# Kernel optimization log

Hardware: AMD Instinct MI355X
Metric: run time of the kernel (lower is better)

## Reference

```python
import jax, jax.numpy as jnp
import numpy as np

B, G, N1, S1 = 2, 16, 4096, 1024
D1, D2 = 128, 256
IN_CH = D1 + D2
MLP = [256, 256]
EPS_DIST = 1e-8
EPS_BN = 1e-5


def setup_inputs() -> dict:
    key = jax.random.key(0)
    ks = jax.random.split(key, 6)
    return {
        "xyz1": jax.random.normal(ks[0], (B, 3, G * N1), jnp.float32),
        "points1": jax.random.normal(ks[1], (B, D1, G * N1), jnp.float32),
        "point_split1": jnp.arange(G + 1, dtype=jnp.int32) * N1,
        "xyz2": jax.random.normal(ks[2], (B, 3, G * S1), jnp.float32),
        "points2": jax.random.normal(ks[3], (B, D2, G * S1), jnp.float32),
        "point_split2": jnp.arange(G + 1, dtype=jnp.int32) * S1,
        "W1": jax.random.normal(ks[4], (MLP[0], IN_CH), jnp.float32) / np.sqrt(IN_CH).astype(np.float32),
        "b1": jnp.zeros((MLP[0],), jnp.float32),
        "gamma1": jnp.ones((MLP[0],), jnp.float32),
        "beta1": jnp.zeros((MLP[0],), jnp.float32),
        "W2": jax.random.normal(ks[5], (MLP[1], MLP[0]), jnp.float32) / np.sqrt(MLP[0]).astype(np.float32),
        "b2": jnp.zeros((MLP[1],), jnp.float32),
        "gamma2": jnp.ones((MLP[1],), jnp.float32),
        "beta2": jnp.zeros((MLP[1],), jnp.float32),
    }


def _bn_relu(x, gamma, beta):
    # training-mode BatchNorm1d over (batch, points) per channel; x: [B, C, N]
    mu = x.mean(axis=(0, 2), keepdims=True)
    var = x.var(axis=(0, 2), keepdims=True)  # biased var, as torch training BN
    xn = (x - mu) * jax.lax.rsqrt(var + EPS_BN)
    return jax.nn.relu(xn * gamma[None, :, None] + beta[None, :, None])


def _fp_segment(x1, x2, p1, p2, W1, b1, g1, be1, W2, b2, g2, be2):
    # x1 [B,3,n], x2 [B,3,s], p1 [B,D1,n], p2 [B,D2,s]
    d = jnp.sum((x1[:, :, :, None] - x2[:, :, None, :]) ** 2, axis=1)  # [B,n,s]
    negd, idx = jax.lax.top_k(-d, 3)  # 3 nearest neighbors
    w = 1.0 / (-negd + EPS_DIST)
    w = w / jnp.sum(w, axis=-1, keepdims=True)  # [B,n,3]

    def gather(p2b, ixb, wb):  # [D2,s], [n,3], [n,3] -> [D2,n]
        return jnp.einsum('dnk,nk->dn', p2b[:, ixb], wb)

    interp = jax.vmap(gather)(p2, idx, w)  # [B,D2,n]
    h = jnp.concatenate([p1, interp], axis=1)  # [B,IN_CH,n]
    h = _bn_relu(jnp.einsum('oc,bcn->bon', W1, h) + b1[None, :, None], g1, be1)
    h = _bn_relu(jnp.einsum('oc,bcn->bon', W2, h) + b2[None, :, None], g2, be2)
    return h  # [B, MLP[-1], n]


def _forward(xyz1, points1, xyz2, points2, W1, b1, gamma1, beta1, W2, b2, gamma2, beta2, g):
    n1 = xyz1.shape[-1] // g
    s1 = xyz2.shape[-1] // g
    seg = lambda t, L: jnp.moveaxis(t.reshape(t.shape[0], t.shape[1], g, L), 2, 0)  # -> [G,B,C,L]
    out = jax.vmap(_fp_segment, in_axes=(0, 0, 0, 0) + (None,) * 8)(
        seg(xyz1, n1), seg(xyz2, s1), seg(points1, n1), seg(points2, s1),
        W1, b1, gamma1, beta1, W2, b2, gamma2, beta2)  # [G,B,C,n1]
    return jnp.moveaxis(out, 0, 2).reshape(out.shape[1], out.shape[2], g * n1)  # [B,C,N]


def reference(xyz1, points1, point_split1, xyz2, points2, point_split2,
              W1, b1, gamma1, beta1, W2, b2, gamma2, beta2):
    g = point_split1.shape[0] - 1  # number of ragged segments (uniform here)
    return _forward(xyz1, points1, xyz2, points2, W1, b1, gamma1, beta1,
                    W2, b2, gamma2, beta2, g)
```

## Files before the change

### kernel.cpp

```cpp
#include <hip/hip_runtime.h>
#include <hip/hip_bf16.h>
#include <hip/hip_fp16.h>

#define B_    2
#define G_    16
#define N_    4096
#define S_    1024
#define D1_   128
#define D2_   256
#define CIN_  384
#define BG_   32
#define GN_   65536
#define GS_   16384

typedef unsigned int u32;
typedef unsigned short u16;
typedef _Float16 f16x8 __attribute__((ext_vector_type(8)));
typedef float f32x4 __attribute__((ext_vector_type(4)));

__device__ __forceinline__ u32 h2bits(__half2 h) { union { __half2 h; u32 u; } c; c.h = h; return c.u; }
__device__ __forceinline__ __half2 bits2h(u32 u) { union { __half2 h; u32 u; } c; c.u = u; return c.h; }
__device__ __forceinline__ u32 pkmax0(u32 v) {
  u32 r; asm("v_pk_max_f16 %0, %1, %2" : "=v"(r) : "v"(v), "v"(0)); return r;
}

#define OFF_W1PK   0u
#define OFF_W2PK   196608u
#define OFF_XYZ2P  327680u
#define OFF_SUM1   851968u
#define OFF_SQ1    868352u
#define OFF_SUM2   884736u
#define OFF_SQ2    901120u
#define OFF_SCPK1  917504u
#define OFF_SHPK1  925696u
#define OFF_SS2    950272u
#define OFF_KNNP   983040u
#define OFF_P2T    5177344u
#define OFF_Y2     21954560u
#define OFF_Y1     122617856u

__launch_bounds__(256)
__global__ void prep_kernel(const float* __restrict__ W1, const float* __restrict__ W2,
                            const float* __restrict__ xyz2,
                            u16* __restrict__ W1pk, u16* __restrict__ W2pk,
                            float4* __restrict__ xyz2p, float* __restrict__ zeros)
{
  int idx = blockIdx.x * 256 + threadIdx.x;
  if (idx < 12288) {
    int lane = idx & 63, ks = (idx >> 6) % 12, mr = idx / (64 * 12);
    int m = mr * 16 + (lane & 15), k = ks * 32 + (lane >> 4) * 8;
    const float* src = W1 + (size_t)m * 384 + k;
    u16* dst = W1pk + (size_t)idx * 8;
    #pragma unroll
    for (int e = 0; e < 8; e++) dst[e] = __half_as_ushort(__float2half_rn(src[e]));
    return;
  }
  idx -= 12288;
  if (idx < 8192) {
    int lane = idx & 63, ks = (idx >> 6) % 8, mr = idx / (64 * 8);
    int m = mr * 16 + (lane & 15), k = ks * 32 + (lane >> 4) * 8;
    const float* src = W2 + (size_t)m * 256 + k;
    u16* dst = W2pk + (size_t)idx * 8;
    #pragma unroll
    for (int e = 0; e < 8; e++) dst[e] = __half_as_ushort(__float2half_rn(src[e]));
    return;
  }
  idx -= 8192;
  if (idx < 16384) { zeros[idx] = 0.f; return; }
  idx -= 16384;
  int bg = idx >> 8, q = idx & 255;
  int b = bg >> 4, g = bg & 15;
  const float* base = xyz2 + (size_t)b * 3 * GS_ + (size_t)g * S_ + q * 4;
  float4 X = *(const float4*)(base);
  float4 Y = *(const float4*)(base + GS_);
  float4 Z = *(const float4*)(base + 2 * GS_);
  float4 M;
  M.x = X.x*X.x + Y.x*Y.x + Z.x*Z.x;
  M.y = X.y*X.y + Y.y*Y.y + Z.y*Z.y;
  M.z = X.z*X.z + Y.z*Y.z + Z.z*Z.z;
  M.w = X.w*X.w + Y.w*Y.w + Z.w*Z.w;
  float4* dst = xyz2p + (size_t)idx * 4;
  dst[0] = X; dst[1] = Y; dst[2] = Z; dst[3] = M;
}

__launch_bounds__(256)
__global__ void t2_kernel(const float* __restrict__ p2, u16* __restrict__ p2T)
{
  __shared__ float tl[64][65];
  int bx = blockIdx.x;
  int bg = bx >> 6, r = bx & 63;
  int ct = r >> 4, st = r & 15;
  int c0 = ct * 64, s0 = st * 64;
  int b = bg >> 4, g = bg & 15;
  int t = threadIdx.x, lane = t & 63, w = t >> 6;
  const float* src = p2 + (size_t)b * D2_ * GS_ + (size_t)g * S_ + s0 + lane;
  #pragma unroll
  for (int i = 0; i < 16; i++) {
    int row = w * 16 + i;
    tl[row][lane] = src[(size_t)(c0 + row) * GS_];
  }
  __syncthreads();
  int cp = t & 31, sr = t >> 5;
  #pragma unroll
  for (int i = 0; i < 8; i++) {
    int sl = sr * 8 + i;
    u32 v = h2bits(__floats2half2_rn(tl[2 * cp][sl], tl[2 * cp + 1][sl]));
    *(u32*)(p2T + (((size_t)bg * 1024 + s0 + sl) * 256 + c0 + 2 * cp)) = v;
  }
}

__launch_bounds__(256)
__global__ void knn_kernel(const float* __restrict__ xyz1, const float4* __restrict__ xyz2p,
                           uint4* __restrict__ knnp)
{
  __shared__ float sd[3][256];
  __shared__ int si[3][256];
  int bx = blockIdx.x;
  int bg = bx >> 6, blk = bx & 63;
  int b = bg >> 4, g = bg & 15;
  int t = threadIdx.x;
  int lane = t & 63, w = t >> 6;
  int n = blk * 64 + lane;
  const float* x1b = xyz1 + (size_t)b * 3 * GN_ + (size_t)g * N_ + n;
  float x = x1b[0], y = x1b[GN_], z = x1b[2 * GN_];
  const float4* xp = xyz2p + (size_t)bg * 1024;

  float d0 = 3.4e38f, d1 = 3.4e38f, d2 = 3.4e38f;
  int i0 = 0, i1 = 0, i2 = 0;
  for (int qq = 0; qq < 64; qq++) {
    int q = w * 64 + qq;
    float4 X = xp[q * 4 + 0], Y = xp[q * 4 + 1], Z = xp[q * 4 + 2], M = xp[q * 4 + 3];
    const float* Xa = (const float*)&X;
    const float* Ya = (const float*)&Y;
    const float* Za = (const float*)&Z;
    const float* Ma = (const float*)&M;
    #pragma unroll
    for (int u = 0; u < 4; u++) {
      float cr = x * Xa[u];
      cr = fmaf(y, Ya[u], cr);
      cr = fmaf(z, Za[u], cr);
      float d = fmaf(-2.f, cr, Ma[u]);
      int s = q * 4 + u;
      bool c2 = d < d2, c1 = d < d1, c0 = d < d0;
      d2 = c1 ? d1 : (c2 ? d : d2);  i2 = c1 ? i1 : (c2 ? s : i2);
      d1 = c0 ? d0 : (c1 ? d : d1);  i1 = c0 ? i0 : (c1 ? s : i1);
      d0 = c0 ? d : d0;              i0 = c0 ? s : i0;
    }
  }

  sd[0][t] = d0; sd[1][t] = d1; sd[2][t] = d2;
  si[0][t] = i0; si[1][t] = i1; si[2][t] = i2;
  __syncthreads();

  if (t < 64) {
    float D0 = d0, D1 = d1, D2 = d2;
    int I0 = i0, I1 = i1, I2 = i2;
    #pragma unroll
    for (int qtr = 1; qtr < 4; qtr++) {
      int idx = qtr * 64 + t;
      #pragma unroll
      for (int c = 0; c < 3; c++) {
        float d = sd[c][idx];
        int s = si[c][idx];
        bool c0 = d < D0, c1 = d < D1, c2 = d < D2;
        I2 = c1 ? I1 : (c2 ? s : I2);  D2 = c1 ? D1 : (c2 ? d : D2);
        I1 = c0 ? I0 : (c1 ? s : I1);  D1 = c0 ? D0 : (c1 ? d : D1);
        I0 = c0 ? s : I0;              D0 = c0 ? d : D0;
      }
    }
    float m1 = x * x + y * y + z * z;
    float t0 = fmaxf(D0 + m1, 0.f), t1 = fmaxf(D1 + m1, 0.f), t2v = fmaxf(D2 + m1, 0.f);
    float w0 = 1.f / (t0 + 1e-8f);
    float w1 = 1.f / (t1 + 1e-8f);
    float w2 = 1.f / (t2v + 1e-8f);
    float inv = 1.f / (w0 + w1 + w2);
    uint4 rec;
    rec.x = h2bits(__floats2half2_rn(w0 * inv, w1 * inv));
    rec.y = (u32)__half_as_ushort(__float2half_rn(w2 * inv));
    rec.z = (u32)I0 | ((u32)I1 << 16);
    rec.w = (u32)I2;
    knnp[(size_t)bg * 4096 + n] = rec;
  }
}

__launch_bounds__(512, 6)
__global__ void gemm1_kernel(const u16* __restrict__ W1pk, const float* __restrict__ points1,
                             const u16* __restrict__ p2T, const uint4* __restrict__ knnp,
                             const float* __restrict__ bias,
                             float* __restrict__ sumw, float* __restrict__ sqw,
                             u16* __restrict__ Y1)
{
  __shared__ __align__(16) char smem[49152];
  int bx = blockIdx.x;
  int bg = bx >> 6, nt = bx & 63;
  int b = bg >> 4, g = bg & 15;
  int n0 = nt * 64;
  int t = threadIdx.x, wid = t >> 6, l = t & 63;
  int llo = l & 15, lhi = l >> 4;

  {
    int r = t >> 3, c4 = t & 7;
    size_t kb = (size_t)bg * 4096 + n0;
    const u16* p2b = p2T + (size_t)bg * 1024 * 256;
    uint4 kp = knnp[kb + r];
    __half2 w0 = __half2half2(__low2half(bits2h(kp.x)));
    __half2 w1 = __half2half2(__high2half(bits2h(kp.x)));
    __half2 w2 = __half2half2(__low2half(bits2h(kp.y)));
    int i0 = kp.z & 0xffff, i1 = kp.z >> 16, i2 = kp.w & 0xffff;
    const u16* r0 = p2b + (size_t)i0 * 256;
    const u16* r1 = p2b + (size_t)i1 * 256;
    const u16* r2 = p2b + (size_t)i2 * 256;
    #pragma unroll
    for (int u = 0; u < 4; u++) {
      int ch = c4 + 8 * u;
      uint4 q0 = *(const uint4*)(r0 + ch * 8);
      uint4 q1 = *(const uint4*)(r1 + ch * 8);
      uint4 q2 = *(const uint4*)(r2 + ch * 8);
      const u32* a0 = (const u32*)&q0;
      const u32* a1 = (const u32*)&q1;
      const u32* a2 = (const u32*)&q2;
      uint4 o;
      u32* ow = (u32*)&o;
      #pragma unroll
      for (int w = 0; w < 4; w++) {
        __half2 v = __hmul2(w2, bits2h(a2[w]));
        v = __hfma2(w1, bits2h(a1[w]), v);
        v = __hfma2(w0, bits2h(a0[w]), v);
        ow[w] = h2bits(v);
      }
      *(uint4*)(smem + r * 768 + ((256 + ch * 16) ^ ((r & 15) << 4))) = o;
    }
    int row = t & 63, chgrp = t >> 6;
    const float* p1c = points1 + ((size_t)b * 128 + chgrp * 16) * (size_t)GN_
                     + (size_t)g * N_ + n0 + row;
    #pragma unroll
    for (int cp = 0; cp < 8; cp++) {
      int c = chgrp * 16 + cp * 2;
      u32 pk = h2bits(__floats2half2_rn(p1c[(size_t)(cp * 2) * GN_],
                                        p1c[(size_t)(cp * 2 + 1) * GN_]));
      *(u32*)(smem + row * 768 + ((c * 2) ^ ((row & 15) << 4))) = pk;
    }
  }
  __syncthreads();

  f32x4 acc[2][4];
  #pragma unroll
  for (int i = 0; i < 2; i++)
    #pragma unroll
    for (int j = 0; j < 4; j++) acc[i][j] = (f32x4)0.f;

  for (int ks = 0; ks < 12; ks++) {
    f16x8 bfr[4], afr[2];
    #pragma unroll
    for (int i = 0; i < 2; i++)
      afr[i] = *(const f16x8*)(W1pk + (size_t)(((wid * 2 + i) * 12 + ks) * 64 + l) * 8);
    #pragma unroll
    for (int j = 0; j < 4; j++) {
      int rb = j * 16 + llo;
      bfr[j] = *(const f16x8*)(smem + rb * 768 + ((ks * 64 + lhi * 16) ^ ((rb & 15) << 4)));
    }
    #pragma unroll
    for (int i = 0; i < 2; i++)
      #pragma unroll
      for (int j = 0; j < 4; j++)
        acc[i][j] = __builtin_amdgcn_mfma_f32_16x16x32_f16(afr[i], bfr[j], acc[i][j], 0, 0, 0);
  }
  __syncthreads();

  #pragma unroll
  for (int i = 0; i < 2; i++) {
    int mloc = wid * 32 + i * 16 + lhi * 4;
    float b0 = bias[mloc], b1 = bias[mloc + 1], b2 = bias[mloc + 2], b3 = bias[mloc + 3];
    float s0 = 0, s1 = 0, s2 = 0, s3 = 0, q0 = 0, q1 = 0, q2 = 0, q3 = 0;
    int slotb = (mloc * 2) & ~15, off8 = (mloc * 2) & 15;
    #pragma unroll
    for (int j = 0; j < 4; j++) {
      int n = j * 16 + llo;
      float v0 = acc[i][j][0] + b0;
      float v1 = acc[i][j][1] + b1;
      float v2 = acc[i][j][2] + b2;
      float v3 = acc[i][j][3] + b3;
      s0 += v0; q0 += v0 * v0;
      s1 += v1; q1 += v1 * v1;
      s2 += v2; q2 += v2 * v2;
      s3 += v3; q3 += v3 * v3;
      int base = n * 512 + (slotb ^ ((n & 7) << 4)) + off8;
      *(u32*)(smem + base) = h2bits(__floats2half2_rn(v0, v1));
      *(u32*)(smem + base + 4) = h2bits(__floats2half2_rn(v2, v3));
    }
    #pragma unroll
    for (int off = 1; off < 16; off <<= 1) {
      s0 += __shfl_xor(s0, off, 64); q0 += __shfl_xor(q0, off, 64);
      s1 += __shfl_xor(s1, off, 64); q1 += __shfl_xor(q1, off, 64);
      s2 += __shfl_xor(s2, off, 64); q2 += __shfl_xor(q2, off, 64);
      s3 += __shfl_xor(s3, off, 64); q3 += __shfl_xor(q3, off, 64);
    }
    if (llo == 0) {
      atomicAdd(&sumw[g * 256 + mloc], s0);     atomicAdd(&sqw[g * 256 + mloc], q0);
      atomicAdd(&sumw[g * 256 + mloc + 1], s1); atomicAdd(&sqw[g * 256 + mloc + 1], q1);
      atomicAdd(&sumw[g * 256 + mloc + 2], s2); atomicAdd(&sqw[g * 256 + mloc + 2], q2);
      atomicAdd(&sumw[g * 256 + mloc + 3], s3); atomicAdd(&sqw[g * 256 + mloc + 3], q3);
    }
  }
  __syncthreads();
  {
    int rn = t >> 3, cq = t & 7;
    u16* yrow = Y1 + ((size_t)bg * 4096 + n0 + rn) * 256;
    #pragma unroll
    for (int u = 0; u < 4; u++) {
      int s = u * 8 + cq;
      uint4 v = *(const uint4*)(smem + rn * 512 + ((s * 16) ^ ((rn & 7) << 4)));
      *(uint4*)(yrow + s * 8) = v;
    }
  }
}

__global__ void bnfin_kernel(const float* __restrict__ sum, const float* __restrict__ sq,
                             const float* __restrict__ gamma, const float* __restrict__ beta,
                             float2* __restrict__ ss, u32* __restrict__ scpk, u32* __restrict__ shpk)
{
  __shared__ float scl[256], shl[256];
  int g = blockIdx.x, m = threadIdx.x;
  int i = g * 256 + m;
  float mean = sum[i] * (1.f / 8192.f);
  float var = sq[i] * (1.f / 8192.f) - mean * mean;
  var = fmaxf(var, 0.f);
  float rstd = rsqrtf(var + 1e-5f);
  float sc = gamma[m] * rstd;
  float sh = beta[m] - mean * sc;
  if (ss) ss[i] = make_float2(sc, sh);
  if (scpk) {
    scl[m] = sc; shl[m] = sh;
    __syncthreads();
    if (m < 128) {
      scpk[g * 128 + m] = h2bits(__floats2half2_rn(scl[2 * m], scl[2 * m + 1]));
      shpk[g * 128 + m] = h2bits(__floats2half2_rn(shl[2 * m], shl[2 * m + 1]));
    }
  }
}

__launch_bounds__(512, 6)
__global__ void gemm2_kernel(const u16* __restrict__ W2pk, const u16* __restrict__ Y1,
                             const u32* __restrict__ scpk, const u32* __restrict__ shpk,
                             const float* __restrict__ bias,
                             float* __restrict__ sumw, float* __restrict__ sqw,
                             u16* __restrict__ Y2)
{
  __shared__ __align__(16) char smem[33792];
  int bx = blockIdx.x;
  int bg = bx >> 6, nt = bx & 63;
  int b = bg >> 4, g = bg & 15;
  int n0 = nt * 64;
  int t = threadIdx.x, wid = t >> 6, l = t & 63;
  int llo = l & 15, lhi = l >> 4;

  if (t < 128) {
    *(u32*)(smem + 32768 + t * 4) = scpk[g * 128 + t];
    *(u32*)(smem + 33280 + t * 4) = shpk[g * 128 + t];
  }

  {
    int rn = t >> 3, qq = t & 7;
    const u16* yrow = Y1 + ((size_t)bg * 4096 + n0 + rn) * 256;
    uint4 sreg[4];
    #pragma unroll
    for (int u = 0; u < 4; u++) sreg[u] = *(const uint4*)(yrow + (qq * 4 + u) * 8);
    __syncthreads();
    const u32* scp = (const u32*)(smem + 32768);
    const u32* shp = (const u32*)(smem + 33280);
    #pragma unroll
    for (int u = 0; u < 4; u++) {
      int s = qq * 4 + u;
      const u32* yw = (const u32*)&sreg[u];
      uint4 o;
      u32* ow = (u32*)&o;
      #pragma unroll
      for (int w = 0; w < 4; w++) {
        int pairi = s * 4 + w;
        __half2 v = __hfma2(bits2h(yw[w]), bits2h(scp[pairi]), bits2h(shp[pairi]));
        ow[w] = pkmax0(h2bits(v));
      }
      *(uint4*)(smem + rn * 512 + ((s * 16) ^ ((rn & 15) << 4))) = o;
    }
  }
  __syncthreads();

  f32x4 acc[2][4];
  #pragma unroll
  for (int i = 0; i < 2; i++)
    #pragma unroll
    for (int j = 0; j < 4; j++) acc[i][j] = (f32x4)0.f;

  for (int ks = 0; ks < 8; ks++) {
    f16x8 bfr[4], afr[2];
    #pragma unroll
    for (int i = 0; i < 2; i++)
      afr[i] = *(const f16x8*)(W2pk + (size_t)(((wid * 2 + i) * 8 + ks) * 64 + l) * 8);
    #pragma unroll
    for (int j = 0; j < 4; j++) {
      int rb = j * 16 + llo;
      bfr[j] = *(const f16x8*)(smem + rb * 512 + ((ks * 64 + lhi * 16) ^ ((rb & 15) << 4)));
    }
    #pragma unroll
    for (int i = 0; i < 2; i++)
      #pragma unroll
      for (int j = 0; j < 4; j++)
        acc[i][j] = __builtin_amdgcn_mfma_f32_16x16x32_f16(afr[i], bfr[j], acc[i][j], 0, 0, 0);
  }
  __syncthreads();

  #pragma unroll
  for (int i = 0; i < 2; i++) {
    int mloc = wid * 32 + i * 16 + lhi * 4;
    float b0 = bias[mloc], b1 = bias[mloc + 1], b2 = bias[mloc + 2], b3 = bias[mloc + 3];
    float s0 = 0, s1 = 0, s2 = 0, s3 = 0, q0 = 0, q1 = 0, q2 = 0, q3 = 0;
    #pragma unroll
    for (int j = 0; j < 4; j++) {
      int n = j * 16 + llo;
      int slotn = (n >> 3) * 16, offn = (n * 2) & 15;
      float v0 = acc[i][j][0] + b0;
      float v1 = acc[i][j][1] + b1;
      float v2 = acc[i][j][2] + b2;
      float v3 = acc[i][j][3] + b3;
      s0 += v0; q0 += v0 * v0;
      s1 += v1; q1 += v1 * v1;
      s2 += v2; q2 += v2 * v2;
      s3 += v3; q3 += v3 * v3;
      *(u16*)(smem + (mloc + 0) * 128 + (slotn ^ (((mloc + 0) & 7) << 4)) + offn) =
          __half_as_ushort(__float2half_rn(v0));
      *(u16*)(smem + (mloc + 1) * 128 + (slotn ^ (((mloc + 1) & 7) << 4)) + offn) =
          __half_as_ushort(__float2half_rn(v1));
      *(u16*)(smem + (mloc + 2) * 128 + (slotn ^ (((mloc + 2) & 7) << 4)) + offn) =
          __half_as_ushort(__float2half_rn(v2));
      *(u16*)(smem + (mloc + 3) * 128 + (slotn ^ (((mloc + 3) & 7) << 4)) + offn) =
          __half_as_ushort(__float2half_rn(v3));
    }
    #pragma unroll
    for (int off = 1; off < 16; off <<= 1) {
      s0 += __shfl_xor(s0, off, 64); q0 += __shfl_xor(q0, off, 64);
      s1 += __shfl_xor(s1, off, 64); q1 += __shfl_xor(q1, off, 64);
      s2 += __shfl_xor(s2, off, 64); q2 += __shfl_xor(q2, off, 64);
      s3 += __shfl_xor(s3, off, 64); q3 += __shfl_xor(q3, off, 64);
    }
    if (llo == 0) {
      atomicAdd(&sumw[g * 256 + mloc], s0);     atomicAdd(&sqw[g * 256 + mloc], q0);
      atomicAdd(&sumw[g * 256 + mloc + 1], s1); atomicAdd(&sqw[g * 256 + mloc + 1], q1);
      atomicAdd(&sumw[g * 256 + mloc + 2], s2); atomicAdd(&sqw[g * 256 + mloc + 2], q2);
      atomicAdd(&sumw[g * 256 + mloc + 3], s3); atomicAdd(&sqw[g * 256 + mloc + 3], q3);
    }
  }
  __syncthreads();
  {
    int mr = t >> 1, hh = t & 1;
    u16* yrow = Y2 + ((size_t)b * 256 + mr) * (size_t)GN_ + (size_t)g * N_ + n0;
    #pragma unroll
    for (int u = 0; u < 4; u++) {
      int s = hh * 4 + u;
      uint4 v = *(const uint4*)(smem + mr * 128 + ((s * 16) ^ ((mr & 7) << 4)));
      *(uint4*)(yrow + s * 8) = v;
    }
  }
}

__launch_bounds__(256)
__global__ void bnapply2_kernel(const u16* __restrict__ Y2, const float2* __restrict__ ss,
                                float* __restrict__ Out)
{
  int f8 = blockIdx.x * 256 + threadIdx.x;
  size_t base = (size_t)f8 * 8;
  int m = (int)((base >> 16) & 255);
  int g = (int)((base >> 12) & 15);
  float2 sc = ss[g * 256 + m];
  uint4 yv = *(const uint4*)(Y2 + base);
  const u32* yw = (const u32*)&yv;
  float4 a, b4;
  float* av = (float*)&a;
  float* bvv = (float*)&b4;
  #pragma unroll
  for (int i = 0; i < 2; i++) {
    float2 f = __half22float2(bits2h(yw[i]));
    av[2 * i]     = fmaxf(fmaf(f.x, sc.x, sc.y), 0.f);
    av[2 * i + 1] = fmaxf(fmaf(f.y, sc.x, sc.y), 0.f);
  }
  #pragma unroll
  for (int i = 0; i < 2; i++) {
    float2 f = __half22float2(bits2h(yw[2 + i]));
    bvv[2 * i]     = fmaxf(fmaf(f.x, sc.x, sc.y), 0.f);
    bvv[2 * i + 1] = fmaxf(fmaf(f.y, sc.x, sc.y), 0.f);
  }
  *(float4*)(Out + base) = a;
  *(float4*)(Out + base + 4) = b4;
}

extern "C" void kernel_launch(void* const* d_in, const int* in_sizes, int n_in,
                              void* d_out, int out_size, void* d_ws, size_t ws_size,
                              hipStream_t stream)
{
  (void)in_sizes; (void)n_in; (void)out_size; (void)ws_size;
  const float* xyz1    = (const float*)d_in[0];
  const float* points1 = (const float*)d_in[1];
  const float* xyz2    = (const float*)d_in[3];
  const float* points2 = (const float*)d_in[4];
  const float* W1      = (const float*)d_in[6];
  const float* b1      = (const float*)d_in[7];
  const float* gamma1  = (const float*)d_in[8];
  const float* beta1   = (const float*)d_in[9];
  const float* W2      = (const float*)d_in[10];
  const float* b2      = (const float*)d_in[11];
  const float* gamma2  = (const float*)d_in[12];
  const float* beta2   = (const float*)d_in[13];
  float* out = (float*)d_out;
  char* ws = (char*)d_ws;

  u16*    W1pk  = (u16*)(ws + OFF_W1PK);
  u16*    W2pk  = (u16*)(ws + OFF_W2PK);
  float4* xyz2p = (float4*)(ws + OFF_XYZ2P);
  float*  sum1  = (float*)(ws + OFF_SUM1);
  float*  sq1   = (float*)(ws + OFF_SQ1);
  float*  sum2  = (float*)(ws + OFF_SUM2);
  float*  sq2   = (float*)(ws + OFF_SQ2);
  u32*    scpk1 = (u32*)(ws + OFF_SCPK1);
  u32*    shpk1 = (u32*)(ws + OFF_SHPK1);
  float2* ss2   = (float2*)(ws + OFF_SS2);
  uint4*  knnp  = (uint4*)(ws + OFF_KNNP);
  u16*    p2T   = (u16*)(ws + OFF_P2T);
  u16*    Y2    = (u16*)(ws + OFF_Y2);
  u16*    Y1    = (u16*)(ws + OFF_Y1);

  prep_kernel<<<176, 256, 0, stream>>>(W1, W2, xyz2, W1pk, W2pk, xyz2p, sum1);
  t2_kernel<<<2048, 256, 0, stream>>>(points2, p2T);
  knn_kernel<<<2048, 256, 0, stream>>>(xyz1, xyz2p, knnp);
  gemm1_kernel<<<2048, 512, 0, stream>>>(W1pk, points1, p2T, knnp, b1, sum1, sq1, Y1);
  bnfin_kernel<<<16, 256, 0, stream>>>(sum1, sq1, gamma1, beta1, nullptr, scpk1, shpk1);
  gemm2_kernel<<<2048, 512, 0, stream>>>(W2pk, Y1, scpk1, shpk1, b2, sum2, sq2, Y2);
  bnfin_kernel<<<16, 256, 0, stream>>>(sum2, sq2, gamma2, beta2, ss2, nullptr, nullptr);
  bnapply2_kernel<<<16384, 256, 0, stream>>>(Y2, ss2, out);
}
```

Measured before the change: 257.2 us.

## Halve GEMM shared-memory footprint by staging K in two halves

Both MLP GEMM kernels now stage the B operand in two K-halves: shared memory is filled with half the input channels, MFMAs run, the buffer is refilled with the other half, and MFMAs run again. The epilogue likewise writes its output tile in two passes through the smaller buffer. This halves LDS per block (48K to 24K and 33K to 17K), which should let more blocks fit on each CU and hide latency better. The cost is extra barriers and serialised gather/transform phases inside each block.

```diff
diff --git a/kernel.cpp b/kernel.cpp
--- a/kernel.cpp
+++ b/kernel.cpp
@@ -190,7 +190,7 @@
                              float* __restrict__ sumw, float* __restrict__ sqw,
                              u16* __restrict__ Y1)
 {
-  __shared__ __align__(16) char smem[49152];
+  __shared__ __align__(16) char smem[24576];
   int bx = blockIdx.x;
   int bg = bx >> 6, nt = bx & 63;
   int b = bg >> 4, g = bg & 15;
@@ -198,38 +198,35 @@
   int t = threadIdx.x, wid = t >> 6, l = t & 63;
   int llo = l & 15, lhi = l >> 4;
 
-  {
-    int r = t >> 3, c4 = t & 7;
-    size_t kb = (size_t)bg * 4096 + n0;
-    const u16* p2b = p2T + (size_t)bg * 1024 * 256;
-    uint4 kp = knnp[kb + r];
+  int gr = t >> 3, c8 = t & 7;
+  const u16* p2b = p2T + (size_t)bg * 1024 * 256;
+  uint4 kp = knnp[(size_t)bg * 4096 + n0 + gr];
+
+  auto interpChunk = [&](int cc, int dstc) {
     __half2 w0 = __half2half2(__low2half(bits2h(kp.x)));
     __half2 w1 = __half2half2(__high2half(bits2h(kp.x)));
     __half2 w2 = __half2half2(__low2half(bits2h(kp.y)));
     int i0 = kp.z & 0xffff, i1 = kp.z >> 16, i2 = kp.w & 0xffff;
-    const u16* r0 = p2b + (size_t)i0 * 256;
-    const u16* r1 = p2b + (size_t)i1 * 256;
-    const u16* r2 = p2b + (size_t)i2 * 256;
-    #pragma unroll
-    for (int u = 0; u < 4; u++) {
-      int ch = c4 + 8 * u;
-      uint4 q0 = *(const uint4*)(r0 + ch * 8);
-      uint4 q1 = *(const uint4*)(r1 + ch * 8);
-      uint4 q2 = *(const uint4*)(r2 + ch * 8);
-      const u32* a0 = (const u32*)&q0;
-      const u32* a1 = (const u32*)&q1;
-      const u32* a2 = (const u32*)&q2;
-      uint4 o;
-      u32* ow = (u32*)&o;
-      #pragma unroll
-      for (int w = 0; w < 4; w++) {
-        __half2 v = __hmul2(w2, bits2h(a2[w]));
-        v = __hfma2(w1, bits2h(a1[w]), v);
-        v = __hfma2(w0, bits2h(a0[w]), v);
-        ow[w] = h2bits(v);
-      }
-      *(uint4*)(smem + r * 768 + ((256 + ch * 16) ^ ((r & 15) << 4))) = o;
-    }
+    uint4 q0 = *(const uint4*)(p2b + (size_t)i0 * 256 + cc * 8);
+    uint4 q1 = *(const uint4*)(p2b + (size_t)i1 * 256 + cc * 8);
+    uint4 q2 = *(const uint4*)(p2b + (size_t)i2 * 256 + cc * 8);
+    const u32* a0 = (const u32*)&q0;
+    const u32* a1 = (const u32*)&q1;
+    const u32* a2 = (const u32*)&q2;
+    uint4 o;
+    u32* ow = (u32*)&o;
+    #pragma unroll
+    for (int w = 0; w < 4; w++) {
+      __half2 v = __hmul2(w2, bits2h(a2[w]));
+      v = __hfma2(w1, bits2h(a1[w]), v);
+      v = __hfma2(w0, bits2h(a0[w]), v);
+      ow[w] = h2bits(v);
+    }
+    *(uint4*)(smem + gr * 384 + (dstc ^ ((gr & 7) << 4))) = o;
+  };
+
+  {
+    interpChunk(c8, 256 + c8 * 16);
     int row = t & 63, chgrp = t >> 6;
     const float* p1c = points1 + ((size_t)b * 128 + chgrp * 16) * (size_t)GN_
                      + (size_t)g * N_ + n0 + row;
@@ -238,7 +235,7 @@
       int c = chgrp * 16 + cp * 2;
       u32 pk = h2bits(__floats2half2_rn(p1c[(size_t)(cp * 2) * GN_],
                                         p1c[(size_t)(cp * 2 + 1) * GN_]));
-      *(u32*)(smem + row * 768 + ((c * 2) ^ ((row & 15) << 4))) = pk;
+      *(u32*)(smem + row * 384 + ((c * 2) ^ ((row & 7) << 4))) = pk;
     }
   }
   __syncthreads();
@@ -249,7 +246,9 @@
     #pragma unroll
     for (int j = 0; j < 4; j++) acc[i][j] = (f32x4)0.f;
 
-  for (int ks = 0; ks < 12; ks++) {
+  #pragma unroll
+  for (int ksl = 0; ksl < 6; ksl++) {
+    int ks = ksl;
     f16x8 bfr[4], afr[2];
     #pragma unroll
     for (int i = 0; i < 2; i++)
@@ -257,7 +256,7 @@
     #pragma unroll
     for (int j = 0; j < 4; j++) {
       int rb = j * 16 + llo;
-      bfr[j] = *(const f16x8*)(smem + rb * 768 + ((ks * 64 + lhi * 16) ^ ((rb & 15) << 4)));
+      bfr[j] = *(const f16x8*)(smem + rb * 384 + ((ksl * 64 + lhi * 16) ^ ((rb & 7) << 4)));
     }
     #pragma unroll
     for (int i = 0; i < 2; i++)
@@ -268,26 +267,88 @@
   __syncthreads();
 
   #pragma unroll
+  for (int u = 0; u < 3; u++) {
+    int cc = 8 + c8 + 8 * u;
+    interpChunk(cc, cc * 16 - 128);
+  }
+  __syncthreads();
+
+  #pragma unroll
+  for (int ksl = 0; ksl < 6; ksl++) {
+    int ks = 6 + ksl;
+    f16x8 bfr[4], afr[2];
+    #pragma unroll
+    for (int i = 0; i < 2; i++)
+      afr[i] = *(const f16x8*)(W1pk + (size_t)(((wid * 2 + i) * 12 + ks) * 64 + l) * 8);
+    #pragma unroll
+    for (int j = 0; j < 4; j++) {
+      int rb = j * 16 + llo;
+      bfr[j] = *(const f16x8*)(smem + rb * 384 + ((ksl * 64 + lhi * 16) ^ ((rb & 7) << 4)));
+    }
+    #pragma unroll
+    for (int i = 0; i < 2; i++)
+      #pragma unroll
+      for (int j = 0; j < 4; j++)
+        acc[i][j] = __builtin_amdgcn_mfma_f32_16x16x32_f16(afr[i], bfr[j], acc[i][j], 0, 0, 0);
+  }
+  __syncthreads();
+
+  float sa[2][4], qa[2][4];
+  #pragma unroll
+  for (int i = 0; i < 2; i++)
+    #pragma unroll
+    for (int r = 0; r < 4; r++) { sa[i][r] = 0.f; qa[i][r] = 0.f; }
+
+  float bv[2][4];
+  #pragma unroll
   for (int i = 0; i < 2; i++) {
     int mloc = wid * 32 + i * 16 + lhi * 4;
-    float b0 = bias[mloc], b1 = bias[mloc + 1], b2 = bias[mloc + 2], b3 = bias[mloc + 3];
-    float s0 = 0, s1 = 0, s2 = 0, s3 = 0, q0 = 0, q1 = 0, q2 = 0, q3 = 0;
-    int slotb = (mloc * 2) & ~15, off8 = (mloc * 2) & 15;
-    #pragma unroll
-    for (int j = 0; j < 4; j++) {
-      int n = j * 16 + llo;
-      float v0 = acc[i][j][0] + b0;
-      float v1 = acc[i][j][1] + b1;
-      float v2 = acc[i][j][2] + b2;
-      float v3 = acc[i][j][3] + b3;
-      s0 += v0; q0 += v0 * v0;
-      s1 += v1; q1 += v1 * v1;
-      s2 += v2; q2 += v2 * v2;
-      s3 += v3; q3 += v3 * v3;
-      int base = n * 512 + (slotb ^ ((n & 7) << 4)) + off8;
-      *(u32*)(smem + base) = h2bits(__floats2half2_rn(v0, v1));
-      *(u32*)(smem + base + 4) = h2bits(__floats2half2_rn(v2, v3));
-    }
+    #pragma unroll
+    for (int r = 0; r < 4; r++) bv[i][r] = bias[mloc + r];
+  }
+
+  #pragma unroll
+  for (int p = 0; p < 2; p++) {
+    #pragma unroll
+    for (int i = 0; i < 2; i++) {
+      int mloc = wid * 32 + i * 16 + lhi * 4;
+      int slotb = (mloc * 2) & ~15, off8 = (mloc * 2) & 15;
+      #pragma unroll
+      for (int j2 = 0; j2 < 2; j2++) {
+        int j = p * 2 + j2;
+        int rn2 = j2 * 16 + llo;
+        float v0 = acc[i][j][0] + bv[i][0];
+        float v1 = acc[i][j][1] + bv[i][1];
+        float v2 = acc[i][j][2] + bv[i][2];
+        float v3 = acc[i][j][3] + bv[i][3];
+        sa[i][0] += v0; qa[i][0] += v0 * v0;
+        sa[i][1] += v1; qa[i][1] += v1 * v1;
+        sa[i][2] += v2; qa[i][2] += v2 * v2;
+        sa[i][3] += v3; qa[i][3] += v3 * v3;
+        int base = rn2 * 512 + (slotb ^ ((rn2 & 7) << 4)) + off8;
+        *(u32*)(smem + base) = h2bits(__floats2half2_rn(v0, v1));
+        *(u32*)(smem + base + 4) = h2bits(__floats2half2_rn(v2, v3));
+      }
+    }
+    __syncthreads();
+    {
+      int rn2 = t >> 4, cq = t & 15;
+      u16* yrow = Y1 + ((size_t)bg * 4096 + n0 + p * 32 + rn2) * 256;
+      #pragma unroll
+      for (int u = 0; u < 2; u++) {
+        int s = u * 16 + cq;
+        uint4 v = *(const uint4*)(smem + rn2 * 512 + ((s * 16) ^ ((rn2 & 7) << 4)));
+        *(uint4*)(yrow + s * 8) = v;
+      }
+    }
+    __syncthreads();
+  }
+
+  #pragma unroll
+  for (int i = 0; i < 2; i++) {
+    int mloc = wid * 32 + i * 16 + lhi * 4;
+    float s0 = sa[i][0], s1 = sa[i][1], s2 = sa[i][2], s3 = sa[i][3];
+    float q0 = qa[i][0], q1 = qa[i][1], q2 = qa[i][2], q3 = qa[i][3];
     #pragma unroll
     for (int off = 1; off < 16; off <<= 1) {
       s0 += __shfl_xor(s0, off, 64); q0 += __shfl_xor(q0, off, 64);
@@ -300,17 +361,6 @@
       atomicAdd(&sumw[g * 256 + mloc + 1], s1); atomicAdd(&sqw[g * 256 + mloc + 1], q1);
       atomicAdd(&sumw[g * 256 + mloc + 2], s2); atomicAdd(&sqw[g * 256 + mloc + 2], q2);
       atomicAdd(&sumw[g * 256 + mloc + 3], s3); atomicAdd(&sqw[g * 256 + mloc + 3], q3);
-    }
-  }
-  __syncthreads();
-  {
-    int rn = t >> 3, cq = t & 7;
-    u16* yrow = Y1 + ((size_t)bg * 4096 + n0 + rn) * 256;
-    #pragma unroll
-    for (int u = 0; u < 4; u++) {
-      int s = u * 8 + cq;
-      uint4 v = *(const uint4*)(smem + rn * 512 + ((s * 16) ^ ((rn & 7) << 4)));
-      *(uint4*)(yrow + s * 8) = v;
     }
   }
 }
@@ -346,7 +396,7 @@
                              float* __restrict__ sumw, float* __restrict__ sqw,
                              u16* __restrict__ Y2)
 {
-  __shared__ __align__(16) char smem[33792];
+  __shared__ __align__(16) char smem[17408];
   int bx = blockIdx.x;
   int bg = bx >> 6, nt = bx & 63;
   int b = bg >> 4, g = bg & 15;
@@ -355,34 +405,35 @@
   int llo = l & 15, lhi = l >> 4;
 
   if (t < 128) {
-    *(u32*)(smem + 32768 + t * 4) = scpk[g * 128 + t];
-    *(u32*)(smem + 33280 + t * 4) = shpk[g * 128 + t];
-  }
-
-  {
-    int rn = t >> 3, qq = t & 7;
-    const u16* yrow = Y1 + ((size_t)bg * 4096 + n0 + rn) * 256;
-    uint4 sreg[4];
-    #pragma unroll
-    for (int u = 0; u < 4; u++) sreg[u] = *(const uint4*)(yrow + (qq * 4 + u) * 8);
-    __syncthreads();
-    const u32* scp = (const u32*)(smem + 32768);
-    const u32* shp = (const u32*)(smem + 33280);
-    #pragma unroll
-    for (int u = 0; u < 4; u++) {
-      int s = qq * 4 + u;
-      const u32* yw = (const u32*)&sreg[u];
+    *(u32*)(smem + 16384 + t * 4) = scpk[g * 128 + t];
+    *(u32*)(smem + 16896 + t * 4) = shpk[g * 128 + t];
+  }
+
+  int rn = t >> 3, qq = t & 7;
+  const u16* yrow0 = Y1 + ((size_t)bg * 4096 + n0 + rn) * 256;
+
+  auto buildB = [&](int h) {
+    const u32* scp = (const u32*)(smem + 16384);
+    const u32* shp = (const u32*)(smem + 16896);
+    #pragma unroll
+    for (int u = 0; u < 2; u++) {
+      int idx = qq * 2 + u;
+      uint4 yv = *(const uint4*)(yrow0 + h * 128 + idx * 8);
+      const u32* yw = (const u32*)&yv;
       uint4 o;
       u32* ow = (u32*)&o;
       #pragma unroll
       for (int w = 0; w < 4; w++) {
-        int pairi = s * 4 + w;
+        int pairi = h * 64 + idx * 4 + w;
         __half2 v = __hfma2(bits2h(yw[w]), bits2h(scp[pairi]), bits2h(shp[pairi]));
         ow[w] = pkmax0(h2bits(v));
       }
-      *(uint4*)(smem + rn * 512 + ((s * 16) ^ ((rn & 15) << 4))) = o;
-    }
-  }
+      *(uint4*)(smem + rn * 256 + ((idx * 16) ^ ((rn & 15) << 4))) = o;
+    }
+  };
+
+  __syncthreads();
+  buildB(0);
   __syncthreads();
 
   f32x4 acc[2][4];
@@ -391,7 +442,9 @@
     #pragma unroll
     for (int j = 0; j < 4; j++) acc[i][j] = (f32x4)0.f;
 
-  for (int ks = 0; ks < 8; ks++) {
+  #pragma unroll
+  for (int ksl = 0; ksl < 4; ksl++) {
+    int ks = ksl;
     f16x8 bfr[4], afr[2];
     #pragma unroll
     for (int i = 0; i < 2; i++)
@@ -399,7 +452,7 @@
     #pragma unroll
     for (int j = 0; j < 4; j++) {
       int rb = j * 16 + llo;
-      bfr[j] = *(const f16x8*)(smem + rb * 512 + ((ks * 64 + lhi * 16) ^ ((rb & 15) << 4)));
+      bfr[j] = *(const f16x8*)(smem + rb * 256 + ((ksl * 64 + lhi * 16) ^ ((rb & 15) << 4)));
     }
     #pragma unroll
     for (int i = 0; i < 2; i++)
@@ -409,32 +462,85 @@
   }
   __syncthreads();
 
+  buildB(1);
+  __syncthreads();
+
+  #pragma unroll
+  for (int ksl = 0; ksl < 4; ksl++) {
+    int ks = 4 + ksl;
+    f16x8 bfr[4], afr[2];
+    #pragma unroll
+    for (int i = 0; i < 2; i++)
+      afr[i] = *(const f16x8*)(W2pk + (size_t)(((wid * 2 + i) * 8 + ks) * 64 + l) * 8);
+    #pragma unroll
+    for (int j = 0; j < 4; j++) {
+      int rb = j * 16 + llo;
+      bfr[j] = *(const f16x8*)(smem + rb * 256 + ((ksl * 64 + lhi * 16) ^ ((rb & 15) << 4)));
+    }
+    #pragma unroll
+    for (int i = 0; i < 2; i++)
+      #pragma unroll
+      for (int j = 0; j < 4; j++)
+        acc[i][j] = __builtin_amdgcn_mfma_f32_16x16x32_f16(afr[i], bfr[j], acc[i][j], 0, 0, 0);
+  }
+  __syncthreads();
+
+  float sa[2][4], qa[2][4];
+  #pragma unroll
+  for (int i = 0; i < 2; i++)
+    #pragma unroll
+    for (int r = 0; r < 4; r++) { sa[i][r] = 0.f; qa[i][r] = 0.f; }
+
+  #pragma unroll
+  for (int p = 0; p < 2; p++) {
+    if ((wid >> 2) == p) {
+      #pragma unroll
+      for (int i = 0; i < 2; i++) {
+        int mloc = wid * 32 + i * 16 + lhi * 4;
+        int mr = mloc - p * 128;
+        float b0 = bias[mloc], b1 = bias[mloc + 1], b2 = bias[mloc + 2], b3 = bias[mloc + 3];
+        #pragma unroll
+        for (int j = 0; j < 4; j++) {
+          int n = j * 16 + llo;
+          int slotn = (n >> 3) * 16, offn = (n * 2) & 15;
+          float v0 = acc[i][j][0] + b0;
+          float v1 = acc[i][j][1] + b1;
+          float v2 = acc[i][j][2] + b2;
+          float v3 = acc[i][j][3] + b3;
+          sa[i][0] += v0; qa[i][0] += v0 * v0;
+          sa[i][1] += v1; qa[i][1] += v1 * v1;
+          sa[i][2] += v2; qa[i][2] += v2 * v2;
+          sa[i][3] += v3; qa[i][3] += v3 * v3;
+          *(u16*)(smem + (mr + 0) * 128 + (slotn ^ (((mr + 0) & 7) << 4)) + offn) =
+              __half_as_ushort(__float2half_rn(v0));
+          *(u16*)(smem + (mr + 1) * 128 + (slotn ^ (((mr + 1) & 7) << 4)) + offn) =
+              __half_as_ushort(__float2half_rn(v1));
+          *(u16*)(smem + (mr + 2) * 128 + (slotn ^ (((mr + 2) & 7) << 4)) + offn) =
+              __half_as_ushort(__float2half_rn(v2));
+          *(u16*)(smem + (mr + 3) * 128 + (slotn ^ (((mr + 3) & 7) << 4)) + offn) =
+              __half_as_ushort(__float2half_rn(v3));
+        }
+      }
+    }
+    __syncthreads();
+    {
+      int mr = t >> 2, cq = t & 3;
+      u16* yrow = Y2 + ((size_t)b * 256 + p * 128 + mr) * (size_t)GN_ + (size_t)g * N_ + n0;
+      #pragma unroll
+      for (int u = 0; u < 2; u++) {
+        int s = cq * 2 + u;
+        uint4 v = *(const uint4*)(smem + mr * 128 + ((s * 16) ^ ((mr & 7) << 4)));
+        *(uint4*)(yrow + s * 8) = v;
+      }
+    }
+    __syncthreads();
+  }
+
   #pragma unroll
   for (int i = 0; i < 2; i++) {
     int mloc = wid * 32 + i * 16 + lhi * 4;
-    float b0 = bias[mloc], b1 = bias[mloc + 1], b2 = bias[mloc + 2], b3 = bias[mloc + 3];
-    float s0 = 0, s1 = 0, s2 = 0, s3 = 0, q0 = 0, q1 = 0, q2 = 0, q3 = 0;
-    #pragma unroll
-    for (int j = 0; j < 4; j++) {
-      int n = j * 16 + llo;
-      int slotn = (n >> 3) * 16, offn = (n * 2) & 15;
-      float v0 = acc[i][j][0] + b0;
-      float v1 = acc[i][j][1] + b1;
-      float v2 = acc[i][j][2] + b2;
-      float v3 = acc[i][j][3] + b3;
-      s0 += v0; q0 += v0 * v0;
-      s1 += v1; q1 += v1 * v1;
-      s2 += v2; q2 += v2 * v2;
-      s3 += v3; q3 += v3 * v3;
-      *(u16*)(smem + (mloc + 0) * 128 + (slotn ^ (((mloc + 0) & 7) << 4)) + offn) =
-          __half_as_ushort(__float2half_rn(v0));
-      *(u16*)(smem + (mloc + 1) * 128 + (slotn ^ (((mloc + 1) & 7) << 4)) + offn) =
-          __half_as_ushort(__float2half_rn(v1));
-      *(u16*)(smem + (mloc + 2) * 128 + (slotn ^ (((mloc + 2) & 7) << 4)) + offn) =
-          __half_as_ushort(__float2half_rn(v2));
-      *(u16*)(smem + (mloc + 3) * 128 + (slotn ^ (((mloc + 3) & 7) << 4)) + offn) =
-          __half_as_ushort(__float2half_rn(v3));
-    }
+    float s0 = sa[i][0], s1 = sa[i][1], s2 = sa[i][2], s3 = sa[i][3];
+    float q0 = qa[i][0], q1 = qa[i][1], q2 = qa[i][2], q3 = qa[i][3];
     #pragma unroll
     for (int off = 1; off < 16; off <<= 1) {
       s0 += __shfl_xor(s0, off, 64); q0 += __shfl_xor(q0, off, 64);
@@ -447,17 +553,6 @@
       atomicAdd(&sumw[g * 256 + mloc + 1], s1); atomicAdd(&sqw[g * 256 + mloc + 1], q1);
       atomicAdd(&sumw[g * 256 + mloc + 2], s2); atomicAdd(&sqw[g * 256 + mloc + 2], q2);
       atomicAdd(&sumw[g * 256 + mloc + 3], s3); atomicAdd(&sqw[g * 256 + mloc + 3], q3);
-    }
-  }
-  __syncthreads();
-  {
-    int mr = t >> 1, hh = t & 1;
-    u16* yrow = Y2 + ((size_t)b * 256 + mr) * (size_t)GN_ + (size_t)g * N_ + n0;
-    #pragma unroll
-    for (int u = 0; u < 4; u++) {
-      int s = hh * 4 + u;
-      uint4 v = *(const uint4*)(smem + mr * 128 + ((s * 16) ^ ((mr & 7) << 4)));
-      *(uint4*)(yrow + s * 8) = v;
     }
   }
 }
```

After: 299.6 us. 16.5% more time.

## Fuse 3-NN search into gemm1 prologue, drop separate knn kernel

Applied to the files above, without the earlier changes.

Removes the standalone knn kernel and computes the three nearest neighbours and interpolation weights inside gemm1's prologue. Each of the 512 threads scans 128 of the 1024 xyz2 candidates for one of 64 rows, and partial top-3 lists are merged through shared memory. This drops a kernel launch and the global write and read of the packed knn records. In exchange, gemm1 gets a heavier serial prologue with extra barriers that cannot overlap with its own MMA work, and register pressure under launch_bounds(512,6) may rise.

```diff
diff --git a/kernel.cpp b/kernel.cpp
--- a/kernel.cpp
+++ b/kernel.cpp
@@ -34,7 +34,6 @@
 #define OFF_SCPK1  917504u
 #define OFF_SHPK1  925696u
 #define OFF_SS2    950272u
-#define OFF_KNNP   983040u
 #define OFF_P2T    5177344u
 #define OFF_Y2     21954560u
 #define OFF_Y1     122617856u
@@ -109,83 +108,10 @@
   }
 }
 
-__launch_bounds__(256)
-__global__ void knn_kernel(const float* __restrict__ xyz1, const float4* __restrict__ xyz2p,
-                           uint4* __restrict__ knnp)
-{
-  __shared__ float sd[3][256];
-  __shared__ int si[3][256];
-  int bx = blockIdx.x;
-  int bg = bx >> 6, blk = bx & 63;
-  int b = bg >> 4, g = bg & 15;
-  int t = threadIdx.x;
-  int lane = t & 63, w = t >> 6;
-  int n = blk * 64 + lane;
-  const float* x1b = xyz1 + (size_t)b * 3 * GN_ + (size_t)g * N_ + n;
-  float x = x1b[0], y = x1b[GN_], z = x1b[2 * GN_];
-  const float4* xp = xyz2p + (size_t)bg * 1024;
-
-  float d0 = 3.4e38f, d1 = 3.4e38f, d2 = 3.4e38f;
-  int i0 = 0, i1 = 0, i2 = 0;
-  for (int qq = 0; qq < 64; qq++) {
-    int q = w * 64 + qq;
-    float4 X = xp[q * 4 + 0], Y = xp[q * 4 + 1], Z = xp[q * 4 + 2], M = xp[q * 4 + 3];
-    const float* Xa = (const float*)&X;
-    const float* Ya = (const float*)&Y;
-    const float* Za = (const float*)&Z;
-    const float* Ma = (const float*)&M;
-    #pragma unroll
-    for (int u = 0; u < 4; u++) {
-      float cr = x * Xa[u];
-      cr = fmaf(y, Ya[u], cr);
-      cr = fmaf(z, Za[u], cr);
-      float d = fmaf(-2.f, cr, Ma[u]);
-      int s = q * 4 + u;
-      bool c2 = d < d2, c1 = d < d1, c0 = d < d0;
-      d2 = c1 ? d1 : (c2 ? d : d2);  i2 = c1 ? i1 : (c2 ? s : i2);
-      d1 = c0 ? d0 : (c1 ? d : d1);  i1 = c0 ? i0 : (c1 ? s : i1);
-      d0 = c0 ? d : d0;              i0 = c0 ? s : i0;
-    }
-  }
-
-  sd[0][t] = d0; sd[1][t] = d1; sd[2][t] = d2;
-  si[0][t] = i0; si[1][t] = i1; si[2][t] = i2;
-  __syncthreads();
-
-  if (t < 64) {
-    float D0 = d0, D1 = d1, D2 = d2;
-    int I0 = i0, I1 = i1, I2 = i2;
-    #pragma unroll
-    for (int qtr = 1; qtr < 4; qtr++) {
-      int idx = qtr * 64 + t;
-      #pragma unroll
-      for (int c = 0; c < 3; c++) {
-        float d = sd[c][idx];
-        int s = si[c][idx];
-        bool c0 = d < D0, c1 = d < D1, c2 = d < D2;
-        I2 = c1 ? I1 : (c2 ? s : I2);  D2 = c1 ? D1 : (c2 ? d : D2);
-        I1 = c0 ? I0 : (c1 ? s : I1);  D1 = c0 ? D0 : (c1 ? d : D1);
-        I0 = c0 ? s : I0;              D0 = c0 ? d : D0;
-      }
-    }
-    float m1 = x * x + y * y + z * z;
-    float t0 = fmaxf(D0 + m1, 0.f), t1 = fmaxf(D1 + m1, 0.f), t2v = fmaxf(D2 + m1, 0.f);
-    float w0 = 1.f / (t0 + 1e-8f);
-    float w1 = 1.f / (t1 + 1e-8f);
-    float w2 = 1.f / (t2v + 1e-8f);
-    float inv = 1.f / (w0 + w1 + w2);
-    uint4 rec;
-    rec.x = h2bits(__floats2half2_rn(w0 * inv, w1 * inv));
-    rec.y = (u32)__half_as_ushort(__float2half_rn(w2 * inv));
-    rec.z = (u32)I0 | ((u32)I1 << 16);
-    rec.w = (u32)I2;
-    knnp[(size_t)bg * 4096 + n] = rec;
-  }
-}
-
 __launch_bounds__(512, 6)
 __global__ void gemm1_kernel(const u16* __restrict__ W1pk, const float* __restrict__ points1,
-                             const u16* __restrict__ p2T, const uint4* __restrict__ knnp,
+                             const u16* __restrict__ p2T, const float* __restrict__ xyz1,
+                             const float4* __restrict__ xyz2p,
                              const float* __restrict__ bias,
                              float* __restrict__ sumw, float* __restrict__ sqw,
                              u16* __restrict__ Y1)
@@ -197,12 +123,75 @@
   int n0 = nt * 64;
   int t = threadIdx.x, wid = t >> 6, l = t & 63;
   int llo = l & 15, lhi = l >> 4;
+  int qr = t >> 3, c8 = t & 7;
 
   {
-    int r = t >> 3, c4 = t & 7;
-    size_t kb = (size_t)bg * 4096 + n0;
+    const float* x1b = xyz1 + (size_t)b * 3 * GN_ + (size_t)g * N_ + n0 + qr;
+    float x = x1b[0], y = x1b[GN_], z = x1b[2 * GN_];
+    const float4* xp = xyz2p + (size_t)bg * 1024;
+    float d0 = 3.4e38f, d1 = 3.4e38f, d2 = 3.4e38f;
+    int i0 = 0, i1 = 0, i2 = 0;
+    for (int k = 0; k < 32; k++) {
+      int qq = c8 * 32 + k;
+      float4 X = xp[qq * 4 + 0], Y = xp[qq * 4 + 1], Z = xp[qq * 4 + 2], M = xp[qq * 4 + 3];
+      const float* Xa = (const float*)&X;
+      const float* Ya = (const float*)&Y;
+      const float* Za = (const float*)&Z;
+      const float* Ma = (const float*)&M;
+      #pragma unroll
+      for (int u = 0; u < 4; u++) {
+        float cr = x * Xa[u];
+        cr = fmaf(y, Ya[u], cr);
+        cr = fmaf(z, Za[u], cr);
+        float d = fmaf(-2.f, cr, Ma[u]);
+        int s = qq * 4 + u;
+        bool cc2 = d < d2, cc1 = d < d1, cc0 = d < d0;
+        d2 = cc1 ? d1 : (cc2 ? d : d2);  i2 = cc1 ? i1 : (cc2 ? s : i2);
+        d1 = cc0 ? d0 : (cc1 ? d : d1);  i1 = cc0 ? i0 : (cc1 ? s : i1);
+        d0 = cc0 ? d : d0;               i0 = cc0 ? s : i0;
+      }
+    }
+    float* sd = (float*)smem;
+    int*   si = (int*)(smem + 6144);
+    sd[0 * 512 + t] = d0; sd[1 * 512 + t] = d1; sd[2 * 512 + t] = d2;
+    si[0 * 512 + t] = i0; si[1 * 512 + t] = i1; si[2 * 512 + t] = i2;
+    __syncthreads();
+    if (c8 == 0) {
+      float D0 = d0, D1 = d1, D2 = d2;
+      int I0 = i0, I1 = i1, I2 = i2;
+      #pragma unroll
+      for (int e = 1; e < 8; e++) {
+        int idx = qr * 8 + e;
+        #pragma unroll
+        for (int c = 0; c < 3; c++) {
+          float d = sd[c * 512 + idx];
+          int s = si[c * 512 + idx];
+          bool cc0 = d < D0, cc1 = d < D1, cc2 = d < D2;
+          I2 = cc1 ? I1 : (cc2 ? s : I2);  D2 = cc1 ? D1 : (cc2 ? d : D2);
+          I1 = cc0 ? I0 : (cc1 ? s : I1);  D1 = cc0 ? D0 : (cc1 ? d : D1);
+          I0 = cc0 ? s : I0;               D0 = cc0 ? d : D0;
+        }
+      }
+      float m1 = x * x + y * y + z * z;
+      float t0 = fmaxf(D0 + m1, 0.f), t1 = fmaxf(D1 + m1, 0.f), t2v = fmaxf(D2 + m1, 0.f);
+      float w0 = 1.f / (t0 + 1e-8f);
+      float w1 = 1.f / (t1 + 1e-8f);
+      float w2 = 1.f / (t2v + 1e-8f);
+      float inv = 1.f / (w0 + w1 + w2);
+      uint4 rec;
+      rec.x = h2bits(__floats2half2_rn(w0 * inv, w1 * inv));
+      rec.y = (u32)__half_as_ushort(__float2half_rn(w2 * inv));
+      rec.z = (u32)I0 | ((u32)I1 << 16);
+      rec.w = (u32)I2;
+      *(uint4*)(smem + 12288 + qr * 16) = rec;
+    }
+    __syncthreads();
+  }
+  uint4 kp = *(const uint4*)(smem + 12288 + qr * 16);
+  __syncthreads();
+
+  {
     const u16* p2b = p2T + (size_t)bg * 1024 * 256;
-    uint4 kp = knnp[kb + r];
     __half2 w0 = __half2half2(__low2half(bits2h(kp.x)));
     __half2 w1 = __half2half2(__high2half(bits2h(kp.x)));
     __half2 w2 = __half2half2(__low2half(bits2h(kp.y)));
@@ -212,7 +201,7 @@
     const u16* r2 = p2b + (size_t)i2 * 256;
     #pragma unroll
     for (int u = 0; u < 4; u++) {
-      int ch = c4 + 8 * u;
+      int ch = c8 + 8 * u;
       uint4 q0 = *(const uint4*)(r0 + ch * 8);
       uint4 q1 = *(const uint4*)(r1 + ch * 8);
       uint4 q2 = *(const uint4*)(r2 + ch * 8);
@@ -228,7 +217,7 @@
         v = __hfma2(w0, bits2h(a0[w]), v);
         ow[w] = h2bits(v);
       }
-      *(uint4*)(smem + r * 768 + ((256 + ch * 16) ^ ((r & 15) << 4))) = o;
+      *(uint4*)(smem + qr * 768 + ((256 + ch * 16) ^ ((qr & 15) << 4))) = o;
     }
     int row = t & 63, chgrp = t >> 6;
     const float* p1c = points1 + ((size_t)b * 128 + chgrp * 16) * (size_t)GN_
@@ -522,15 +511,13 @@
   u32*    scpk1 = (u32*)(ws + OFF_SCPK1);
   u32*    shpk1 = (u32*)(ws + OFF_SHPK1);
   float2* ss2   = (float2*)(ws + OFF_SS2);
-  uint4*  knnp  = (uint4*)(ws + OFF_KNNP);
   u16*    p2T   = (u16*)(ws + OFF_P2T);
   u16*    Y2    = (u16*)(ws + OFF_Y2);
   u16*    Y1    = (u16*)(ws + OFF_Y1);
 
   prep_kernel<<<176, 256, 0, stream>>>(W1, W2, xyz2, W1pk, W2pk, xyz2p, sum1);
   t2_kernel<<<2048, 256, 0, stream>>>(points2, p2T);
-  knn_kernel<<<2048, 256, 0, stream>>>(xyz1, xyz2p, knnp);
-  gemm1_kernel<<<2048, 512, 0, stream>>>(W1pk, points1, p2T, knnp, b1, sum1, sq1, Y1);
+  gemm1_kernel<<<2048, 512, 0, stream>>>(W1pk, points1, p2T, xyz1, xyz2p, b1, sum1, sq1, Y1);
   bnfin_kernel<<<16, 256, 0, stream>>>(sum1, sq1, gamma1, beta1, nullptr, scpk1, shpk1);
   gemm2_kernel<<<2048, 512, 0, stream>>>(W2pk, Y1, scpk1, shpk1, b2, sum2, sq2, Y2);
   bnfin_kernel<<<16, 256, 0, stream>>>(sum2, sq2, gamma2, beta2, ss2, nullptr, nullptr);
```

After: 391.2 us. 1.52x slower.
